# Optimization experiments

Measured on AMD Instinct MI355X. Metric: run time of the kernel, lower is better.

Reference implementation:

```python
import jax, jax.numpy as jnp
import numpy as np

HIDDEN = 256
ITEM_SIZE = 50000
SEQ_LEN = 256
BATCH = 256
ALPHA = 0.2      # LeakyReLU negative slope
LN_EPS = 1e-12


def setup_inputs() -> dict:
    key = jax.random.key(0)
    ks = jax.random.split(key, 8)
    item_seq = jax.random.randint(ks[0], (BATCH, SEQ_LEN), 0, ITEM_SIZE)
    item_emb_table = 0.02 * jax.random.normal(ks[1], (ITEM_SIZE, HIDDEN), dtype=jnp.float32)
    item_emb_table = item_emb_table.at[0].set(0.0)  # padding_idx=0
    pos_emb_table = 0.02 * jax.random.normal(ks[2], (SEQ_LEN, HIDDEN), dtype=jnp.float32)
    W = 0.02 * jax.random.normal(ks[3], (HIDDEN, HIDDEN), dtype=jnp.float32)  # stored [in,out]
    a1 = 0.02 * jax.random.normal(ks[4], (HIDDEN,), dtype=jnp.float32)  # a weight, first half (acts on h_i)
    a2 = 0.02 * jax.random.normal(ks[5], (HIDDEN,), dtype=jnp.float32)  # second half (acts on h_j)
    gamma = jnp.ones((HIDDEN,), dtype=jnp.float32)
    beta = jnp.zeros((HIDDEN,), dtype=jnp.float32)
    return {"item_seq": item_seq, "item_emb_table": item_emb_table,
            "pos_emb_table": pos_emb_table, "W": W, "a1": a1, "a2": a2,
            "gamma": gamma, "beta": beta}


def _layernorm(x, gamma, beta):
    mu = jnp.mean(x, axis=-1, keepdims=True)
    var = jnp.mean(jnp.square(x - mu), axis=-1, keepdims=True)
    return (x - mu) * jax.lax.rsqrt(var + LN_EPS) * gamma + beta


def reference(item_seq, item_emb_table, pos_emb_table, W, a1, a2, gamma, beta):
    B, L = item_seq.shape
    x = item_emb_table[item_seq] + pos_emb_table[jnp.arange(L)][None, :, :]  # [B,L,H]
    x = _layernorm(x, gamma, beta)
    # dropout is identity at eval time
    h = jnp.einsum('blh,hk->blk', x, W)  # GAT W projection, [B,L,H]
    # a([h_i ; h_j]) = a1.h_i + a2.h_j  -> rank-1 separable scores (same math, no O(L^2 H) concat)
    s1 = h @ a1  # [B,L]
    s2 = h @ a2  # [B,L]
    e = jax.nn.leaky_relu(s1[:, :, None] + s2[:, None, :], negative_slope=ALPHA)  # [B,L,L]
    # adj is all-ones, so the -9e15 mask is a no-op
    attn = jax.nn.softmax(e, axis=-1)
    return jnp.einsum('bij,bjh->bih', attn, h)  # [B,L,H]
```

## Files before the change

### kernel.cpp

```cpp
#include <hip/hip_runtime.h>
#include <hip/hip_bf16.h>

#define ALPHA  0.2f
#define L2E    1.4426950408889634f

typedef __attribute__((ext_vector_type(8))) short  short8;
typedef __attribute__((ext_vector_type(4))) float  f32x4;
typedef unsigned short u16;

__device__ __forceinline__ u16 f2bf(float f) {
    union { float f; unsigned int u; } v; v.f = f;
    unsigned int r = (v.u + 0x7FFFu + ((v.u >> 16) & 1u)) >> 16;
    return (u16)r;
}
__device__ __forceinline__ float lrelu(float x) { return fmaxf(x, ALPHA * x); }
__device__ __forceinline__ unsigned pk2(float a, float b) {
    return (unsigned)f2bf(a) | ((unsigned)f2bf(b) << 16);
}

__global__ void prep(const float* __restrict__ W, const float* __restrict__ a1,
                     const float* __restrict__ a2, u16* __restrict__ wfrag,
                     float* __restrict__ w1, float* __restrict__ w2) {
    int b = blockIdx.x;
    if (b < 64) {
        int t    = threadIdx.x;
        int pair = b * 2 + (t >> 7);
        int l    = (t >> 1) & 63;
        int jh   = (t & 1) * 4;
        int ks   = pair >> 4, cb = pair & 15;
        int c  = cb * 16 + (l & 15);
        int k0 = ks * 32 + (l >> 4) * 8 + jh;
        ushort4 o;
        o.x = f2bf(W[(size_t)(k0 + 0) * 256 + c]);
        o.y = f2bf(W[(size_t)(k0 + 1) * 256 + c]);
        o.z = f2bf(W[(size_t)(k0 + 2) * 256 + c]);
        o.w = f2bf(W[(size_t)(k0 + 3) * 256 + c]);
        *(ushort4*)&wfrag[(size_t)pair * 512 + l * 8 + jh] = o;
    } else {
        int bb = b - 64;
        int wv = threadIdx.x >> 6, lane = threadIdx.x & 63;
        for (int kk = 0; kk < 16; ++kk) {
            int k = bb * 64 + wv * 16 + kk;
            float4 wv4 = *(const float4*)(W + (size_t)k * 256 + 4 * lane);
            float4 a14 = *(const float4*)(a1 + 4 * lane);
            float4 a24 = *(const float4*)(a2 + 4 * lane);
            float d1 = wv4.x*a14.x + wv4.y*a14.y + wv4.z*a14.z + wv4.w*a14.w;
            float d2 = wv4.x*a24.x + wv4.y*a24.y + wv4.z*a24.z + wv4.w*a24.w;
            #pragma unroll
            for (int off = 32; off; off >>= 1) {
                d1 += __shfl_xor(d1, off);
                d2 += __shfl_xor(d2, off);
            }
            if (lane == 0) { w1[k] = d1; w2[k] = d2; }
        }
    }
}

__global__ __launch_bounds__(1024)
void gat(const int* __restrict__ item_seq, const float* __restrict__ emb,
         const float* __restrict__ pos, const float* __restrict__ gamma,
         const float* __restrict__ beta, const float* __restrict__ w1,
         const float* __restrict__ w2, const u16* __restrict__ wfrag,
         float* __restrict__ out)
{
    __shared__ u16 xb[256 * 256];
    __shared__ __align__(16) float s1s[256], s2s[256], mS[256];
    __shared__ __align__(16) float part[256][4];
    __shared__ float wmax[16];
    const int b    = blockIdx.x;
    const int tid  = threadIdx.x;
    const int lane = tid & 63, wid = tid >> 6, g = lane >> 4, li = lane & 15;
    const int iw_  = wid >> 2, nw = wid & 3;

    {
        float4 g4  = *(const float4*)(gamma + 4 * lane);
        float4 b4  = *(const float4*)(beta  + 4 * lane);
        float4 w14 = *(const float4*)(w1    + 4 * lane);
        float4 w24 = *(const float4*)(w2    + 4 * lane);
        float4 u4, t4;
        u4.x = g4.x*w14.x; u4.y = g4.y*w14.y; u4.z = g4.z*w14.z; u4.w = g4.w*w14.w;
        t4.x = g4.x*w24.x; t4.y = g4.y*w24.y; t4.z = g4.z*w24.z; t4.w = g4.w*w24.w;
        float cA = u4.x + u4.y + u4.z + u4.w;
        float cB = t4.x + t4.y + t4.z + t4.w;
        float cC = b4.x*w14.x + b4.y*w14.y + b4.z*w14.z + b4.w*w14.w;
        float cD = b4.x*w24.x + b4.y*w24.y + b4.z*w24.z + b4.w*w24.w;
        #pragma unroll
        for (int off = 32; off; off >>= 1) {
            cA += __shfl_xor(cA, off); cB += __shfl_xor(cB, off);
            cC += __shfl_xor(cC, off); cD += __shfl_xor(cD, off);
        }
        float rm = -3.0e38f;
        #pragma unroll 2
        for (int it = 0; it < 8; ++it) {
            int rA = it * 32 + wid, rB = rA + 16;
            int gA = item_seq[b * 256 + rA];
            int gB = item_seq[b * 256 + rB];
            float4 eA = *(const float4*)(emb + (size_t)gA * 256 + 4 * lane);
            float4 pA = *(const float4*)(pos + (size_t)rA * 256 + 4 * lane);
            float4 eB = *(const float4*)(emb + (size_t)gB * 256 + 4 * lane);
            float4 pB = *(const float4*)(pos + (size_t)rB * 256 + 4 * lane);
            float4 vA, vB;
            vA.x = eA.x + pA.x; vA.y = eA.y + pA.y; vA.z = eA.z + pA.z; vA.w = eA.w + pA.w;
            vB.x = eB.x + pB.x; vB.y = eB.y + pB.y; vB.z = eB.z + pB.z; vB.w = eB.w + pB.w;
            float sa = vA.x + vA.y + vA.z + vA.w;
            float qa = vA.x*vA.x + vA.y*vA.y + vA.z*vA.z + vA.w*vA.w;
            float d1a = vA.x*u4.x + vA.y*u4.y + vA.z*u4.z + vA.w*u4.w;
            float d2a = vA.x*t4.x + vA.y*t4.y + vA.z*t4.z + vA.w*t4.w;
            float sb = vB.x + vB.y + vB.z + vB.w;
            float qb = vB.x*vB.x + vB.y*vB.y + vB.z*vB.z + vB.w*vB.w;
            float d1b = vB.x*u4.x + vB.y*u4.y + vB.z*u4.z + vB.w*u4.w;
            float d2b = vB.x*t4.x + vB.y*t4.y + vB.z*t4.z + vB.w*t4.w;
            #pragma unroll
            for (int off = 32; off; off >>= 1) {
                sa  += __shfl_xor(sa,  off);  sb  += __shfl_xor(sb,  off);
                qa  += __shfl_xor(qa,  off);  qb  += __shfl_xor(qb,  off);
                d1a += __shfl_xor(d1a, off);  d1b += __shfl_xor(d1b, off);
                d2a += __shfl_xor(d2a, off);  d2b += __shfl_xor(d2b, off);
            }
            float muA = sa * (1.0f/256.0f);
            float rsA = rsqrtf(qa * (1.0f/256.0f) - muA*muA + 1e-12f);
            float muB = sb * (1.0f/256.0f);
            float rsB = rsqrtf(qb * (1.0f/256.0f) - muB*muB + 1e-12f);
            float s1A = rsA * (d1a - muA * cA) + cC;
            float s2A = rsA * (d2a - muA * cB) + cD;
            float s1B = rsB * (d1b - muB * cA) + cC;
            float s2B = rsB * (d2b - muB * cB) + cD;
            if (lane == 0) {
                s1s[rA] = s1A; s2s[rA] = s2A;
                s1s[rB] = s1B; s2s[rB] = s2B;
            }
            rm = fmaxf(rm, fmaxf(s2A, s2B));
            ushort4 oA, oB;
            oA.x = f2bf((vA.x - muA) * rsA * g4.x + b4.x);
            oA.y = f2bf((vA.y - muA) * rsA * g4.y + b4.y);
            oA.z = f2bf((vA.z - muA) * rsA * g4.z + b4.z);
            oA.w = f2bf((vA.w - muA) * rsA * g4.w + b4.w);
            oB.x = f2bf((vB.x - muB) * rsB * g4.x + b4.x);
            oB.y = f2bf((vB.y - muB) * rsB * g4.y + b4.y);
            oB.z = f2bf((vB.z - muB) * rsB * g4.z + b4.z);
            oB.w = f2bf((vB.w - muB) * rsB * g4.w + b4.w);
            int sl = (lane >> 1), sub = (lane & 1) * 4;
            *(ushort4*)&xb[rA * 256 + ((sl ^ (rA & 7)) << 3) + sub] = oA;
            *(ushort4*)&xb[rB * 256 + ((sl ^ (rB & 7)) << 3) + sub] = oB;
        }
        if (lane == 0) wmax[wid] = rm;
    }
    __syncthreads();

    {
        float s2m = wmax[0];
        #pragma unroll
        for (int k = 1; k < 16; ++k) s2m = fmaxf(s2m, wmax[k]);
        int i = tid >> 2, jq = tid & 3;
        float s1v = s1s[i];
        float mi  = lrelu(s1v + s2m);
        float sum = 0.f;
        const float4* sp = (const float4*)&s2s[jq * 64];
        #pragma unroll 4
        for (int j4 = 0; j4 < 16; ++j4) {
            float4 sv = sp[j4];
            sum += __builtin_amdgcn_exp2f((lrelu(s1v + sv.x) - mi) * L2E);
            sum += __builtin_amdgcn_exp2f((lrelu(s1v + sv.y) - mi) * L2E);
            sum += __builtin_amdgcn_exp2f((lrelu(s1v + sv.z) - mi) * L2E);
            sum += __builtin_amdgcn_exp2f((lrelu(s1v + sv.w) - mi) * L2E);
        }
        if (jq == 0) mS[i] = mi;
        part[i][jq] = sum;
    }

    f32x4 acc[4][4];
    #pragma unroll
    for (int mt = 0; mt < 4; ++mt)
        #pragma unroll
        for (int nt = 0; nt < 4; ++nt)
            acc[mt][nt] = (f32x4){0.f, 0.f, 0.f, 0.f};

    #pragma unroll
    for (int ks = 0; ks < 8; ++ks) {
        short8 bf[4];
        #pragma unroll
        for (int nt = 0; nt < 4; ++nt)
            bf[nt] = *(const short8*)(wfrag
                       + ((size_t)(ks * 16 + nw * 4 + nt) * 64 + lane) * 8);
        #pragma unroll
        for (int mt = 0; mt < 4; ++mt) {
            int rl = iw_ * 64 + mt * 16 + li;
            short8 af = *(const short8*)&xb[rl * 256 + (((ks*4+g) ^ (rl & 7)) << 3)];
            #pragma unroll
            for (int nt = 0; nt < 4; ++nt)
                acc[mt][nt] = __builtin_amdgcn_mfma_f32_16x16x32_bf16(
                    af, bf[nt], acc[mt][nt], 0, 0, 0);
        }
    }
    __syncthreads();

    #pragma unroll
    for (int mt = 0; mt < 4; ++mt)
        #pragma unroll
        for (int nt = 0; nt < 4; ++nt) {
            int c  = nw * 64 + nt * 16 + li;
            int i0 = iw_ * 64 + mt * 16 + 4 * g;
            uint2 o;
            o.x = pk2(acc[mt][nt][0], acc[mt][nt][1]);
            o.y = pk2(acc[mt][nt][2], acc[mt][nt][3]);
            *(uint2*)&xb[c * 256 + (((i0 >> 3) ^ (c & 7)) << 3) + (i0 & 7)] = o;
        }
    __syncthreads();

    {
        f32x4 oacc[4][4];
        #pragma unroll
        for (int mt = 0; mt < 4; ++mt)
            #pragma unroll
            for (int nt = 0; nt < 4; ++nt)
                oacc[mt][nt] = (f32x4){0.f, 0.f, 0.f, 0.f};

        float s1r[4], mv[4], lv[4];
        #pragma unroll
        for (int mt = 0; mt < 4; ++mt) {
            int i = iw_ * 64 + mt * 16 + li;
            s1r[mt] = s1s[i];
            mv[mt]  = mS[i];
            lv[mt]  = 1.0f / (part[i][0] + part[i][1] + part[i][2] + part[i][3]);
        }

        #pragma unroll
        for (int js = 0; js < 8; ++js) {
            float s2l[8];
            #pragma unroll
            for (int jj = 0; jj < 8; ++jj) s2l[jj] = s2s[js * 32 + g * 8 + jj];

            short8 pfr[4];
            #pragma unroll
            for (int mt = 0; mt < 4; ++mt) {
                union { unsigned int u[4]; short8 s; } pk;
                #pragma unroll
                for (int q2 = 0; q2 < 4; ++q2) {
                    float e0 = lrelu(s1r[mt] + s2l[2 * q2]);
                    float e1 = lrelu(s1r[mt] + s2l[2 * q2 + 1]);
                    float p0 = __builtin_amdgcn_exp2f((e0 - mv[mt]) * L2E) * lv[mt];
                    float p1 = __builtin_amdgcn_exp2f((e1 - mv[mt]) * L2E) * lv[mt];
                    pk.u[q2] = pk2(p0, p1);
                }
                pfr[mt] = pk.s;
            }
            #pragma unroll
            for (int nt = 0; nt < 4; ++nt) {
                int cl = nw * 64 + nt * 16 + li;
                short8 vf = *(const short8*)&xb[cl * 256
                              + (((js * 4 + g) ^ (cl & 7)) << 3)];
                #pragma unroll
                for (int mt = 0; mt < 4; ++mt)
                    oacc[mt][nt] = __builtin_amdgcn_mfma_f32_16x16x32_bf16(
                        pfr[mt], vf, oacc[mt][nt], 0, 0, 0);
            }
        }

        size_t ob = (size_t)b * (256 * 256);
        #pragma unroll
        for (int mt = 0; mt < 4; ++mt)
            #pragma unroll
            for (int nt = 0; nt < 4; ++nt) {
                int c  = nw * 64 + nt * 16 + li;
                int i0 = iw_ * 64 + mt * 16 + 4 * g;
                #pragma unroll
                for (int q2 = 0; q2 < 4; ++q2)
                    out[ob + (size_t)(i0 + q2) * 256 + c] = oacc[mt][nt][q2];
            }
    }
}

extern "C" void kernel_launch(void* const* d_in, const int* in_sizes, int n_in,
                              void* d_out, int out_size, void* d_ws, size_t ws_size,
                              hipStream_t stream) {
    (void)in_sizes; (void)n_in; (void)out_size; (void)ws_size;
    const int*   seq   = (const int*)d_in[0];
    const float* emb   = (const float*)d_in[1];
    const float* pos   = (const float*)d_in[2];
    const float* W     = (const float*)d_in[3];
    const float* a1    = (const float*)d_in[4];
    const float* a2    = (const float*)d_in[5];
    const float* gamma = (const float*)d_in[6];
    const float* beta  = (const float*)d_in[7];

    char* ws = (char*)d_ws;
    u16*   wfrag = (u16*)ws;
    float* w1    = (float*)(ws + 131072);
    float* w2    = (float*)(ws + 132096);

    hipLaunchKernelGGL(prep, dim3(68), dim3(256), 0, stream, W, a1, a2, wfrag, w1, w2);
    hipLaunchKernelGGL(gat, dim3(256), dim3(1024), 0, stream,
                       seq, emb, pos, gamma, beta, w1, w2, wfrag, (float*)d_out);
}
```

Baseline: 70.77 us.

## Prescale scores by log2e, fold softmax normalizer into exponent, retile PV warps

Attention scores are pre-multiplied by log2(e) and the softmax max and log-sum are folded into per-row constants. Each probability then costs one add, one fma, a max and an exp2, with no subtract, multiply or normalize. The P·V stage is retiled from 4x4 to 2x8 MFMA tiles per warp, so each warp computes half as many probability fragments per step but reads more V fragments. LayerNorm outputs are also packed with pk2. Folding the normalizer into the exponent via log2 slightly changes rounding.

```diff
diff --git a/kernel.cpp b/kernel.cpp
--- a/kernel.cpp
+++ b/kernel.cpp
@@ -13,10 +13,10 @@
     unsigned int r = (v.u + 0x7FFFu + ((v.u >> 16) & 1u)) >> 16;
     return (u16)r;
 }
-__device__ __forceinline__ float lrelu(float x) { return fmaxf(x, ALPHA * x); }
 __device__ __forceinline__ unsigned pk2(float a, float b) {
     return (unsigned)f2bf(a) | ((unsigned)f2bf(b) << 16);
 }
+__device__ __forceinline__ float lrelu(float x) { return fmaxf(x, ALPHA * x); }
 
 __global__ void prep(const float* __restrict__ W, const float* __restrict__ a1,
                      const float* __restrict__ a2, u16* __restrict__ wfrag,
@@ -121,27 +121,27 @@
             float rsA = rsqrtf(qa * (1.0f/256.0f) - muA*muA + 1e-12f);
             float muB = sb * (1.0f/256.0f);
             float rsB = rsqrtf(qb * (1.0f/256.0f) - muB*muB + 1e-12f);
-            float s1A = rsA * (d1a - muA * cA) + cC;
-            float s2A = rsA * (d2a - muA * cB) + cD;
-            float s1B = rsB * (d1b - muB * cA) + cC;
-            float s2B = rsB * (d2b - muB * cB) + cD;
+            float s1A = (rsA * (d1a - muA * cA) + cC) * L2E;
+            float s2A = (rsA * (d2a - muA * cB) + cD) * L2E;
+            float s1B = (rsB * (d1b - muB * cA) + cC) * L2E;
+            float s2B = (rsB * (d2b - muB * cB) + cD) * L2E;
             if (lane == 0) {
                 s1s[rA] = s1A; s2s[rA] = s2A;
                 s1s[rB] = s1B; s2s[rB] = s2B;
             }
             rm = fmaxf(rm, fmaxf(s2A, s2B));
-            ushort4 oA, oB;
-            oA.x = f2bf((vA.x - muA) * rsA * g4.x + b4.x);
-            oA.y = f2bf((vA.y - muA) * rsA * g4.y + b4.y);
-            oA.z = f2bf((vA.z - muA) * rsA * g4.z + b4.z);
-            oA.w = f2bf((vA.w - muA) * rsA * g4.w + b4.w);
-            oB.x = f2bf((vB.x - muB) * rsB * g4.x + b4.x);
-            oB.y = f2bf((vB.y - muB) * rsB * g4.y + b4.y);
-            oB.z = f2bf((vB.z - muB) * rsB * g4.z + b4.z);
-            oB.w = f2bf((vB.w - muB) * rsB * g4.w + b4.w);
+            uint2 oA, oB;
+            oA.x = pk2((vA.x - muA) * rsA * g4.x + b4.x,
+                       (vA.y - muA) * rsA * g4.y + b4.y);
+            oA.y = pk2((vA.z - muA) * rsA * g4.z + b4.z,
+                       (vA.w - muA) * rsA * g4.w + b4.w);
+            oB.x = pk2((vB.x - muB) * rsB * g4.x + b4.x,
+                       (vB.y - muB) * rsB * g4.y + b4.y);
+            oB.y = pk2((vB.z - muB) * rsB * g4.z + b4.z,
+                       (vB.w - muB) * rsB * g4.w + b4.w);
             int sl = (lane >> 1), sub = (lane & 1) * 4;
-            *(ushort4*)&xb[rA * 256 + ((sl ^ (rA & 7)) << 3) + sub] = oA;
-            *(ushort4*)&xb[rB * 256 + ((sl ^ (rB & 7)) << 3) + sub] = oB;
+            *(uint2*)&xb[rA * 256 + ((sl ^ (rA & 7)) << 3) + sub] = oA;
+            *(uint2*)&xb[rB * 256 + ((sl ^ (rB & 7)) << 3) + sub] = oB;
         }
         if (lane == 0) wmax[wid] = rm;
     }
@@ -154,15 +154,17 @@
         int i = tid >> 2, jq = tid & 3;
         float s1v = s1s[i];
         float mi  = lrelu(s1v + s2m);
+        float aB0 = s1v - mi;
+        float bB0 = ALPHA * s1v - mi;
         float sum = 0.f;
         const float4* sp = (const float4*)&s2s[jq * 64];
         #pragma unroll 4
         for (int j4 = 0; j4 < 16; ++j4) {
             float4 sv = sp[j4];
-            sum += __builtin_amdgcn_exp2f((lrelu(s1v + sv.x) - mi) * L2E);
-            sum += __builtin_amdgcn_exp2f((lrelu(s1v + sv.y) - mi) * L2E);
-            sum += __builtin_amdgcn_exp2f((lrelu(s1v + sv.z) - mi) * L2E);
-            sum += __builtin_amdgcn_exp2f((lrelu(s1v + sv.w) - mi) * L2E);
+            sum += __builtin_amdgcn_exp2f(fmaxf(aB0 + sv.x, fmaf(ALPHA, sv.x, bB0)));
+            sum += __builtin_amdgcn_exp2f(fmaxf(aB0 + sv.y, fmaf(ALPHA, sv.y, bB0)));
+            sum += __builtin_amdgcn_exp2f(fmaxf(aB0 + sv.z, fmaf(ALPHA, sv.z, bB0)));
+            sum += __builtin_amdgcn_exp2f(fmaxf(aB0 + sv.w, fmaf(ALPHA, sv.w, bB0)));
         }
         if (jq == 0) mS[i] = mi;
         part[i][jq] = sum;
@@ -208,49 +210,54 @@
     __syncthreads();
 
     {
-        f32x4 oacc[4][4];
-        #pragma unroll
-        for (int mt = 0; mt < 4; ++mt)
-            #pragma unroll
-            for (int nt = 0; nt < 4; ++nt)
+        const int ig2 = wid >> 1;
+        const int ng2 = wid & 1;
+        f32x4 oacc[2][8];
+        #pragma unroll
+        for (int mt = 0; mt < 2; ++mt)
+            #pragma unroll
+            for (int nt = 0; nt < 8; ++nt)
                 oacc[mt][nt] = (f32x4){0.f, 0.f, 0.f, 0.f};
 
-        float s1r[4], mv[4], lv[4];
-        #pragma unroll
-        for (int mt = 0; mt < 4; ++mt) {
-            int i = iw_ * 64 + mt * 16 + li;
-            s1r[mt] = s1s[i];
-            mv[mt]  = mS[i];
-            lv[mt]  = 1.0f / (part[i][0] + part[i][1] + part[i][2] + part[i][3]);
+        float aBase[2], bBase[2];
+        #pragma unroll
+        for (int mt = 0; mt < 2; ++mt) {
+            int i = ig2 * 32 + mt * 16 + li;
+            float lsum = part[i][0] + part[i][1] + part[i][2] + part[i][3];
+            float Mi = mS[i] + __log2f(lsum);
+            float s1v = s1s[i];
+            aBase[mt] = s1v - Mi;
+            bBase[mt] = ALPHA * s1v - Mi;
         }
 
         #pragma unroll
         for (int js = 0; js < 8; ++js) {
-            float s2l[8];
-            #pragma unroll
-            for (int jj = 0; jj < 8; ++jj) s2l[jj] = s2s[js * 32 + g * 8 + jj];
-
-            short8 pfr[4];
-            #pragma unroll
-            for (int mt = 0; mt < 4; ++mt) {
+            float4 sv0 = *(const float4*)&s2s[js * 32 + g * 8];
+            float4 sv1 = *(const float4*)&s2s[js * 32 + g * 8 + 4];
+            float s2l[8] = {sv0.x, sv0.y, sv0.z, sv0.w, sv1.x, sv1.y, sv1.z, sv1.w};
+
+            short8 pfr[2];
+            #pragma unroll
+            for (int mt = 0; mt < 2; ++mt) {
                 union { unsigned int u[4]; short8 s; } pk;
                 #pragma unroll
                 for (int q2 = 0; q2 < 4; ++q2) {
-                    float e0 = lrelu(s1r[mt] + s2l[2 * q2]);
-                    float e1 = lrelu(s1r[mt] + s2l[2 * q2 + 1]);
-                    float p0 = __builtin_amdgcn_exp2f((e0 - mv[mt]) * L2E) * lv[mt];
-                    float p1 = __builtin_amdgcn_exp2f((e1 - mv[mt]) * L2E) * lv[mt];
+                    float sA = s2l[2 * q2], sB = s2l[2 * q2 + 1];
+                    float p0 = __builtin_amdgcn_exp2f(
+                        fmaxf(aBase[mt] + sA, fmaf(ALPHA, sA, bBase[mt])));
+                    float p1 = __builtin_amdgcn_exp2f(
+                        fmaxf(aBase[mt] + sB, fmaf(ALPHA, sB, bBase[mt])));
                     pk.u[q2] = pk2(p0, p1);
                 }
                 pfr[mt] = pk.s;
             }
             #pragma unroll
-            for (int nt = 0; nt < 4; ++nt) {
-                int cl = nw * 64 + nt * 16 + li;
+            for (int nt = 0; nt < 8; ++nt) {
+                int cl = ng2 * 128 + nt * 16 + li;
                 short8 vf = *(const short8*)&xb[cl * 256
                               + (((js * 4 + g) ^ (cl & 7)) << 3)];
                 #pragma unroll
-                for (int mt = 0; mt < 4; ++mt)
+                for (int mt = 0; mt < 2; ++mt)
                     oacc[mt][nt] = __builtin_amdgcn_mfma_f32_16x16x32_bf16(
                         pfr[mt], vf, oacc[mt][nt], 0, 0, 0);
             }
@@ -258,11 +265,11 @@
 
         size_t ob = (size_t)b * (256 * 256);
         #pragma unroll
-        for (int mt = 0; mt < 4; ++mt)
-            #pragma unroll
-            for (int nt = 0; nt < 4; ++nt) {
-                int c  = nw * 64 + nt * 16 + li;
-                int i0 = iw_ * 64 + mt * 16 + 4 * g;
+        for (int mt = 0; mt < 2; ++mt)
+            #pragma unroll
+            for (int nt = 0; nt < 8; ++nt) {
+                int c  = ng2 * 128 + nt * 16 + li;
+                int i0 = ig2 * 32 + mt * 16 + 4 * g;
                 #pragma unroll
                 for (int q2 = 0; q2 < 4; ++q2)
                     out[ob + (size_t)(i0 + q2) * 256 + c] = oacc[mt][nt][q2];
```

Result: faster. 60.33 us (-14.7%).
